# Optimization experiments

Measured on AMD Instinct MI355X. Metric: run time of the kernel, lower is better.

Reference implementation:

```python
import jax, jax.numpy as jnp
import numpy as np

B, S, D = 2, 2048, 1024
H = 16
HD = D // H

def setup_inputs() -> dict:
    key = jax.random.key(0)
    ks = jax.random.split(key, 9)
    s = 1.0 / np.sqrt(D)
    return {
        "x": jax.random.normal(ks[0], (B, S, D), dtype=jnp.float32),
        "Wq": jax.random.normal(ks[1], (D, D), dtype=jnp.float32) * s,
        "bq": jnp.zeros((D,), dtype=jnp.float32),
        "Wk": jax.random.normal(ks[2], (D, D), dtype=jnp.float32) * s,
        "bk": jnp.zeros((D,), dtype=jnp.float32),
        "Wv": jax.random.normal(ks[3], (D, D), dtype=jnp.float32) * s,
        "bv": jnp.zeros((D,), dtype=jnp.float32),
        "Wo": jax.random.normal(ks[4], (D, D), dtype=jnp.float32) * s,
        "bo": jnp.zeros((D,), dtype=jnp.float32),
    }

def reference(x, Wq, bq, Wk, bk, Wv, bv, Wo, bo):
    b, s, d = x.shape
    # torch Linear: y = x @ W.T + b
    def proj(W, bias):
        y = jnp.einsum('bsd,ed->bse', x, W) + bias
        return y.reshape(b, s, H, HD).transpose(0, 2, 1, 3)  # [b,h,s,hd]
    Q = proj(Wq, bq)
    K = proj(Wk, bk)
    V = proj(Wv, bv)
    scale = 1.0 / jnp.sqrt(jnp.float32(HD))
    scores = jnp.einsum('bhqd,bhkd->bhqk', Q, K) * scale  # [b,h,s,s]
    attn = jax.nn.softmax(scores, axis=-1)
    out = jnp.einsum('bhqk,bhkd->bhqd', attn, V)  # [b,h,s,hd]
    out = out.transpose(0, 2, 1, 3).reshape(b, s, d)
    return jnp.einsum('bsd,ed->bse', out, Wo) + bo
```

## Files before the change

kernel.cpp:

```cpp
#include <hip/hip_runtime.h>
#include <stdint.h>


typedef __bf16 bf16x8 __attribute__((ext_vector_type(8)));
typedef float  f32x4  __attribute__((ext_vector_type(4)));
typedef unsigned short u16x8 __attribute__((ext_vector_type(8)));

#define LOG2E 1.44269504088896f
#define FIXED_MAX_BITS 14.4269504088896f

__device__ __forceinline__ unsigned short f2bf(float f) {
    union { float f; unsigned u; } v; v.f = f;
    unsigned r = v.u + 0x7FFFu + ((v.u >> 16) & 1u);
    return (unsigned short)(r >> 16);
}
__device__ __forceinline__ float bf2f(unsigned short u) {
    union { unsigned u; float f; } v; v.u = (unsigned)u << 16; return v.f;
}

__device__ __forceinline__ float exp2_fast(float x) {
#if __has_builtin(__builtin_amdgcn_exp2f)
    return __builtin_amdgcn_exp2f(x);
#else
    return __expf(x * 0.69314718056f);
#endif
}

__device__ __forceinline__ void glds16(const void* g, void* l) {
    __builtin_amdgcn_global_load_lds(
        (__attribute__((address_space(1))) void*)(g),
        (__attribute__((address_space(3))) void*)(l),
        16, 0, 0);
}

__global__ __launch_bounds__(256) void cvt_all(
    const float* __restrict__ x,  const float* __restrict__ Wq,
    const float* __restrict__ Wk, const float* __restrict__ Wv,
    const float* __restrict__ Wo,
    unsigned short* __restrict__ xb,  unsigned short* __restrict__ Wqb,
    unsigned short* __restrict__ Wkb, unsigned short* __restrict__ Wvb,
    unsigned short* __restrict__ Wob)
{
    const int stride = gridDim.x * blockDim.x;
    for (int i = blockIdx.x * blockDim.x + threadIdx.x; i < 2097152; i += stride) {
        const float* src; unsigned short* dst; int j;
        if (i < 1048576) { src = x; dst = xb; j = i; }
        else {
            int t = (i - 1048576) >> 18; j = (i - 1048576) & 262143;
            src = (t == 0) ? Wq : (t == 1) ? Wk : (t == 2) ? Wv : Wo;
            dst = (t == 0) ? Wqb : (t == 1) ? Wkb : (t == 2) ? Wvb : Wob;
        }
        float4 v = ((const float4*)src)[j];
        ushort4 o;
        o.x = f2bf(v.x); o.y = f2bf(v.y); o.z = f2bf(v.z); o.w = f2bf(v.w);
        ((ushort4*)dst)[j] = o;
    }
}

template <int MODE>
__global__ __launch_bounds__(256) void gemm_bt(
    const unsigned short* __restrict__ A,
    const unsigned short* __restrict__ W0,
    const unsigned short* __restrict__ W1,
    const unsigned short* __restrict__ W2,
    const float* __restrict__ b0,
    const float* __restrict__ b1,
    const float* __restrict__ b2,
    unsigned short* __restrict__ outQ,
    unsigned short* __restrict__ outK,
    unsigned short* __restrict__ outV,
    float* __restrict__ outF)
{
    constexpr int BM = (MODE == 0) ? 128 : 64;
    constexpr int FM = BM / 32;
    constexpr int RA = BM / 32;

    __shared__ __attribute__((aligned(16))) unsigned short As[BM * 64];
    __shared__ __attribute__((aligned(16))) unsigned short Bs[128 * 64];

    const int tid  = threadIdx.x;
    const int lane = tid & 63;
    const int wid  = tid >> 6;
    const int quad = lane >> 4;
    const int l16  = lane & 15;

    const int m0 = blockIdx.x * BM;

    const unsigned short* W;
    const float* bias;
    int proj, n0;
    if (MODE == 0) {
        proj = blockIdx.y >> 3;
        n0   = (blockIdx.y & 7) * 128;
        W    = (proj == 0) ? W0 : (proj == 1) ? W1 : W2;
        bias = (proj == 0) ? b0 : (proj == 1) ? b1 : b2;
    } else {
        proj = 0;
        n0   = blockIdx.y * 128;
        W    = W0;
        bias = b0;
    }

    const int wm = (wid >> 1) * (BM / 2);
    const int wn = (wid & 1) * 64;

    f32x4 acc[FM][4];
#pragma unroll
    for (int i = 0; i < FM; ++i)
#pragma unroll
        for (int j = 0; j < 4; ++j)
            acc[i][j] = (f32x4){0.f, 0.f, 0.f, 0.f};

    char* AsB  = (char*)As;
    char* BsB  = (char*)Bs;
    char* ldsA = AsB + wid * 1024;
    char* ldsB = BsB + wid * 1024;

    for (int k0 = 0; k0 < 1024; k0 += 64) {
#pragma unroll
        for (int q = 0; q < RA; ++q) {
            int i   = q * 256 + tid;
            int row = i >> 3;
            int sc  = (i & 7) ^ (row & 7);
            glds16(A + (size_t)(m0 + row) * 1024 + k0 + sc * 8, ldsA + q * 4096);
        }
#pragma unroll
        for (int q = 0; q < 4; ++q) {
            int i   = q * 256 + tid;
            int row = i >> 3;
            int sc  = (i & 7) ^ (row & 7);
            glds16(W + (size_t)(n0 + row) * 1024 + k0 + sc * 8, ldsB + q * 4096);
        }
        __syncthreads();

#pragma unroll
        for (int kh = 0; kh < 2; ++kh) {
            bf16x8 af[FM], bfr[4];
#pragma unroll
            for (int t = 0; t < FM; ++t) {
                int r = wm + t * 16 + l16;
                int c = (kh * 4 + quad) ^ (r & 7);
                af[t] = *(const bf16x8*)(AsB + r * 128 + c * 16);
            }
#pragma unroll
            for (int t = 0; t < 4; ++t) {
                int r = wn + t * 16 + l16;
                int c = (kh * 4 + quad) ^ (r & 7);
                bfr[t] = *(const bf16x8*)(BsB + r * 128 + c * 16);
            }
#pragma unroll
            for (int i = 0; i < FM; ++i)
#pragma unroll
                for (int j = 0; j < 4; ++j)
                    acc[i][j] = __builtin_amdgcn_mfma_f32_16x16x32_bf16(
                        af[i], bfr[j], acc[i][j], 0, 0, 0);
        }
        __syncthreads();
    }

#pragma unroll
    for (int i = 0; i < FM; ++i) {
        const int mrow0 = m0 + wm + i * 16 + quad * 4;
#pragma unroll
        for (int j = 0; j < 4; ++j) {
            const int n  = n0 + wn + j * 16 + l16;
            const float bb = bias[n];
            if (MODE == 1) {
#pragma unroll
                for (int r = 0; r < 4; ++r)
                    outF[(size_t)(mrow0 + r) * 1024 + n] = acc[i][j][r] + bb;
            } else {
                const int h = n >> 6, hd = n & 63;
                if (proj == 2) {
                    const int b = mrow0 >> 11, s = mrow0 & 2047;
                    ushort4 pk;
                    pk.x = f2bf(acc[i][j][0] + bb);
                    pk.y = f2bf(acc[i][j][1] + bb);
                    pk.z = f2bf(acc[i][j][2] + bb);
                    pk.w = f2bf(acc[i][j][3] + bb);
                    *(ushort4*)(outV + ((size_t)((b * 16 + h) * 64 + hd)) * 2048 + s) = pk;
                } else {
                    unsigned short* dst = (proj == 0) ? outQ : outK;
                    const float scl = (proj == 0) ? (0.125f * LOG2E) : 1.0f;
#pragma unroll
                    for (int r = 0; r < 4; ++r) {
                        const int m = mrow0 + r;
                        const int b = m >> 11, s = m & 2047;
                        dst[((size_t)((b * 16 + h) * 2048 + s)) * 64 + hd] =
                            f2bf((acc[i][j][r] + bb) * scl);
                    }
                }
            }
        }
    }
}

__global__ __launch_bounds__(256, 4) void attn_kernel(
    const unsigned short* __restrict__ Qb,
    const unsigned short* __restrict__ Kb,
    const unsigned short* __restrict__ Vtb,
    unsigned short* __restrict__ OP,
    float* __restrict__ LS)
{
    __shared__ __attribute__((aligned(16))) unsigned short Ks[128 * 64];
    __shared__ __attribute__((aligned(16))) unsigned short Vs[2 * 64 * 64];

    const int tid  = threadIdx.x;
    const int lane = tid & 63;
    const int wid  = tid >> 6;
    const int quad = lane >> 4;
    const int l16  = lane & 15;
    const int l7   = l16 & 7;

    const int half = blockIdx.x & 1;
    const int q0   = (blockIdx.x >> 1) * 128 + wid * 32;
    const int hb   = blockIdx.y;
    const int bq   = hb >> 4, hh = hb & 15;

    const unsigned short* Qh  = Qb  + (size_t)hb * 2048 * 64;
    const unsigned short* Kh  = Kb  + (size_t)hb * 2048 * 64;
    const unsigned short* Vth = Vtb + (size_t)hb * 64 * 2048;

    bf16x8 qf[2][2];
#pragma unroll
    for (int qt = 0; qt < 2; ++qt) {
        const unsigned short* qp = Qh + (size_t)(q0 + qt * 16 + l16) * 64 + quad * 8;
        qf[qt][0] = *(const bf16x8*)(qp);
        qf[qt][1] = *(const bf16x8*)(qp + 32);
    }

    f32x4 o[4][2];
#pragma unroll
    for (int ht = 0; ht < 4; ++ht)
#pragma unroll
        for (int qt = 0; qt < 2; ++qt)
            o[ht][qt] = (f32x4){0.f, 0.f, 0.f, 0.f};
    float lsum[2] = {0.f, 0.f};

    char* KsB  = (char*)Ks;
    char* ldsK = KsB + wid * 1024;

    const int base_row = 8 * (l16 >> 2) + (l16 & 3);
    const int kp0 = ((quad) ^ l7) * 16;
    const int kp1 = ((4 + quad) ^ l7) * 16;
    const int vrow = l16 * 128;

    const int kc0 = half * 1024;
    for (int kc = kc0; kc < kc0 + 1024; kc += 128) {
#pragma unroll
        for (int q = 0; q < 4; ++q) {
            int i   = q * 256 + tid;
            int row = i >> 3;
            int g   = (row & 3) | (((row >> 3) & 1) << 2);
            int ch  = (i & 7) ^ g;
            glds16(Kh + (size_t)(kc + row) * 64 + ch * 8, ldsK + q * 4096);
        }
#pragma unroll
        for (int sub = 0; sub < 2; ++sub)
#pragma unroll
            for (int q = 0; q < 2; ++q) {
                int i   = q * 256 + tid;
                int row = i >> 3;
                int ch  = (i & 7) ^ (row & 7);
                glds16(Vth + (size_t)row * 2048 + kc + sub * 64 + ch * 8,
                       (char*)Vs + sub * 8192 + wid * 1024 + q * 4096);
            }
        __syncthreads();

#pragma unroll
        for (int st32 = 0; st32 < 4; ++st32) {
            const char* krb = KsB + (st32 * 32 + base_row) * 128;
            bf16x8 kf00 = *(const bf16x8*)(krb + kp0);
            bf16x8 kf01 = *(const bf16x8*)(krb + kp1);
            bf16x8 kf10 = *(const bf16x8*)(krb + 512 + kp0);
            bf16x8 kf11 = *(const bf16x8*)(krb + 512 + kp1);

            const f32x4 mi = (f32x4){-FIXED_MAX_BITS, -FIXED_MAX_BITS,
                                     -FIXED_MAX_BITS, -FIXED_MAX_BITS};
            f32x4 s00 = mi, s01 = mi, s10 = mi, s11 = mi;
            s00 = __builtin_amdgcn_mfma_f32_16x16x32_bf16(kf00, qf[0][0], s00, 0, 0, 0);
            s00 = __builtin_amdgcn_mfma_f32_16x16x32_bf16(kf01, qf[0][1], s00, 0, 0, 0);
            s01 = __builtin_amdgcn_mfma_f32_16x16x32_bf16(kf10, qf[0][0], s01, 0, 0, 0);
            s01 = __builtin_amdgcn_mfma_f32_16x16x32_bf16(kf11, qf[0][1], s01, 0, 0, 0);
            s10 = __builtin_amdgcn_mfma_f32_16x16x32_bf16(kf00, qf[1][0], s10, 0, 0, 0);
            s10 = __builtin_amdgcn_mfma_f32_16x16x32_bf16(kf01, qf[1][1], s10, 0, 0, 0);
            s11 = __builtin_amdgcn_mfma_f32_16x16x32_bf16(kf10, qf[1][0], s11, 0, 0, 0);
            s11 = __builtin_amdgcn_mfma_f32_16x16x32_bf16(kf11, qf[1][1], s11, 0, 0, 0);

            bf16x8 p8[2];
#pragma unroll
            for (int qt = 0; qt < 2; ++qt) {
                const f32x4 sA = qt ? s10 : s00;
                const f32x4 sB = qt ? s11 : s01;
                float e0 = exp2_fast(sA[0]), e1 = exp2_fast(sA[1]);
                float e2 = exp2_fast(sA[2]), e3 = exp2_fast(sA[3]);
                float e4 = exp2_fast(sB[0]), e5 = exp2_fast(sB[1]);
                float e6 = exp2_fast(sB[2]), e7 = exp2_fast(sB[3]);
                lsum[qt] += ((e0 + e1) + (e2 + e3)) + ((e4 + e5) + (e6 + e7));
                u16x8 up;
                up[0] = f2bf(e0); up[1] = f2bf(e1); up[2] = f2bf(e2); up[3] = f2bf(e3);
                up[4] = f2bf(e4); up[5] = f2bf(e5); up[6] = f2bf(e6); up[7] = f2bf(e7);
                p8[qt] = __builtin_bit_cast(bf16x8, up);
            }

            const int voff = (st32 >> 1) * 8192 + vrow
                           + ((((st32 & 1) * 4 + quad) ^ l7) * 16);
#pragma unroll
            for (int ht = 0; ht < 4; ++ht) {
                const bf16x8 vf = *(const bf16x8*)((char*)Vs + voff + ht * 2048);
                o[ht][0] = __builtin_amdgcn_mfma_f32_16x16x32_bf16(vf, p8[0], o[ht][0], 0, 0, 0);
                o[ht][1] = __builtin_amdgcn_mfma_f32_16x16x32_bf16(vf, p8[1], o[ht][1], 0, 0, 0);
            }
        }
        __syncthreads();
    }

    float lt[2];
#pragma unroll
    for (int qt = 0; qt < 2; ++qt) {
        float s = lsum[qt];
        s += __shfl_xor(s, 16);
        s += __shfl_xor(s, 32);
        lt[qt] = s;
    }

    unsigned short* OPh = OP + (size_t)half * 4096 * 1024;
#pragma unroll
    for (int qt = 0; qt < 2; ++qt) {
        const size_t row = (size_t)(bq * 2048 + q0 + qt * 16 + l16);
#pragma unroll
        for (int ht = 0; ht < 4; ++ht) {
            ushort4 pk;
            pk.x = f2bf(o[ht][qt][0]);
            pk.y = f2bf(o[ht][qt][1]);
            pk.z = f2bf(o[ht][qt][2]);
            pk.w = f2bf(o[ht][qt][3]);
            *(ushort4*)(OPh + row * 1024 + hh * 64 + ht * 16 + quad * 4) = pk;
        }
    }
    if (quad == 0) {
        LS[half * 65536 + hb * 2048 + q0 + l16]      = lt[0];
        LS[half * 65536 + hb * 2048 + q0 + 16 + l16] = lt[1];
    }
}

__global__ __launch_bounds__(256) void attn_reduce(
    const unsigned short* __restrict__ OP,
    const float* __restrict__ LS,
    unsigned short* __restrict__ attnb)
{
    const size_t idx = ((size_t)blockIdx.x * 256 + threadIdx.x) * 8;
    const int row = (int)(idx >> 10);
    const int col = (int)(idx & 1023);
    const int bh  = ((row >> 11) << 4) + (col >> 6);
    const int q   = row & 2047;
    const float l = LS[bh * 2048 + q] + LS[65536 + bh * 2048 + q];
    const float rl = 1.0f / l;

    ushort4 a0 = *(const ushort4*)(OP + idx);
    ushort4 a1 = *(const ushort4*)(OP + idx + 4);
    ushort4 b0 = *(const ushort4*)(OP + 4194304 + idx);
    ushort4 b1 = *(const ushort4*)(OP + 4194304 + idx + 4);
    ushort4 o0, o1;
    o0.x = f2bf((bf2f(a0.x) + bf2f(b0.x)) * rl);
    o0.y = f2bf((bf2f(a0.y) + bf2f(b0.y)) * rl);
    o0.z = f2bf((bf2f(a0.z) + bf2f(b0.z)) * rl);
    o0.w = f2bf((bf2f(a0.w) + bf2f(b0.w)) * rl);
    o1.x = f2bf((bf2f(a1.x) + bf2f(b1.x)) * rl);
    o1.y = f2bf((bf2f(a1.y) + bf2f(b1.y)) * rl);
    o1.z = f2bf((bf2f(a1.z) + bf2f(b1.z)) * rl);
    o1.w = f2bf((bf2f(a1.w) + bf2f(b1.w)) * rl);
    *(ushort4*)(attnb + idx)     = o0;
    *(ushort4*)(attnb + idx + 4) = o1;
}

extern "C" void kernel_launch(void* const* d_in, const int* in_sizes, int n_in,
                              void* d_out, int out_size, void* d_ws, size_t ws_size,
                              hipStream_t stream) {
    (void)in_sizes; (void)n_in; (void)out_size; (void)ws_size;

    const float* x  = (const float*)d_in[0];
    const float* Wq = (const float*)d_in[1];
    const float* bq = (const float*)d_in[2];
    const float* Wk = (const float*)d_in[3];
    const float* bk = (const float*)d_in[4];
    const float* Wv = (const float*)d_in[5];
    const float* bv = (const float*)d_in[6];
    const float* Wo = (const float*)d_in[7];
    const float* bo = (const float*)d_in[8];

    char* ws = (char*)d_ws;
    const size_t MB = 1024 * 1024;
    unsigned short* xb    = (unsigned short*)(ws + 0);
    unsigned short* Wqb   = (unsigned short*)(ws + 8  * MB);
    unsigned short* Wkb   = (unsigned short*)(ws + 10 * MB);
    unsigned short* Wvb   = (unsigned short*)(ws + 12 * MB);
    unsigned short* Wob   = (unsigned short*)(ws + 14 * MB);
    unsigned short* Qb    = (unsigned short*)(ws + 16 * MB);
    unsigned short* Kb    = (unsigned short*)(ws + 24 * MB);
    unsigned short* Vtb   = (unsigned short*)(ws + 32 * MB);
    unsigned short* attnb = (unsigned short*)(ws + 40 * MB);
    unsigned short* OP    = (unsigned short*)(ws + 48 * MB);
    float*          LSb   = (float*)(ws + 64 * MB);

    cvt_all<<<dim3(1024), dim3(256), 0, stream>>>(
        x, Wq, Wk, Wv, Wo, xb, Wqb, Wkb, Wvb, Wob);

    gemm_bt<0><<<dim3(32, 24), dim3(256), 0, stream>>>(
        xb, Wqb, Wkb, Wvb, bq, bk, bv, Qb, Kb, Vtb, nullptr);

    attn_kernel<<<dim3(32, 32), dim3(256), 0, stream>>>(Qb, Kb, Vtb, OP, LSb);

    attn_reduce<<<dim3(2048), dim3(256), 0, stream>>>(OP, LSb, attnb);

    gemm_bt<1><<<dim3(64, 8), dim3(256), 0, stream>>>(
        attnb, Wob, nullptr, nullptr, bo, nullptr, nullptr,
        nullptr, nullptr, nullptr, (float*)d_out);
}
```

Measured before the change: 199.1 us.

## Fuse x fp32-to-bf16 conversion into QKV GEMM and use packed bf16 converts

Drops the separate conversion of x to bf16. The QKV GEMM now loads fp32 x directly, converts it in registers and stores it to LDS, which removes one full write and read of the activation through HBM. It also replaces scalar bf16 rounding with the packed cvt_pk_bf16_f32 builtin where available, in the attention softmax, in the epilogues and in the reduce. In exchange, the A operand in the QKV GEMM is now loaded synchronously through registers instead of async global_load_lds, and each x tile is converted repeatedly, once per N-block (24 column blocks).

```diff
diff --git a/kernel.cpp b/kernel.cpp
--- a/kernel.cpp
+++ b/kernel.cpp
@@ -3,8 +3,9 @@
 
 
 typedef __bf16 bf16x8 __attribute__((ext_vector_type(8)));
+typedef __bf16 bf16x2 __attribute__((ext_vector_type(2)));
 typedef float  f32x4  __attribute__((ext_vector_type(4)));
-typedef unsigned short u16x8 __attribute__((ext_vector_type(8)));
+typedef unsigned int u32x4v __attribute__((ext_vector_type(4)));
 
 #define LOG2E 1.44269504088896f
 #define FIXED_MAX_BITS 14.4269504088896f
@@ -16,6 +17,14 @@
 }
 __device__ __forceinline__ float bf2f(unsigned short u) {
     union { unsigned u; float f; } v; v.u = (unsigned)u << 16; return v.f;
+}
+
+__device__ __forceinline__ unsigned cvtpk(float a, float b) {
+#if __has_builtin(__builtin_amdgcn_cvt_pk_bf16_f32)
+    return __builtin_bit_cast(unsigned, __builtin_amdgcn_cvt_pk_bf16_f32(a, b));
+#else
+    return (unsigned)f2bf(a) | ((unsigned)f2bf(b) << 16);
+#endif
 }
 
 __device__ __forceinline__ float exp2_fast(float x) {
@@ -33,33 +42,29 @@
         16, 0, 0);
 }
 
-__global__ __launch_bounds__(256) void cvt_all(
-    const float* __restrict__ x,  const float* __restrict__ Wq,
-    const float* __restrict__ Wk, const float* __restrict__ Wv,
-    const float* __restrict__ Wo,
-    unsigned short* __restrict__ xb,  unsigned short* __restrict__ Wqb,
-    unsigned short* __restrict__ Wkb, unsigned short* __restrict__ Wvb,
-    unsigned short* __restrict__ Wob)
+__global__ __launch_bounds__(256) void cvt_w(
+    const float* __restrict__ Wq, const float* __restrict__ Wk,
+    const float* __restrict__ Wv, const float* __restrict__ Wo,
+    unsigned short* __restrict__ Wqb, unsigned short* __restrict__ Wkb,
+    unsigned short* __restrict__ Wvb, unsigned short* __restrict__ Wob)
 {
     const int stride = gridDim.x * blockDim.x;
-    for (int i = blockIdx.x * blockDim.x + threadIdx.x; i < 2097152; i += stride) {
-        const float* src; unsigned short* dst; int j;
-        if (i < 1048576) { src = x; dst = xb; j = i; }
-        else {
-            int t = (i - 1048576) >> 18; j = (i - 1048576) & 262143;
-            src = (t == 0) ? Wq : (t == 1) ? Wk : (t == 2) ? Wv : Wo;
-            dst = (t == 0) ? Wqb : (t == 1) ? Wkb : (t == 2) ? Wvb : Wob;
-        }
+    for (int i = blockIdx.x * blockDim.x + threadIdx.x; i < 1048576; i += stride) {
+        int t = i >> 18, j = i & 262143;
+        const float* src = (t == 0) ? Wq : (t == 1) ? Wk : (t == 2) ? Wv : Wo;
+        unsigned short* dst = (t == 0) ? Wqb : (t == 1) ? Wkb : (t == 2) ? Wvb : Wob;
         float4 v = ((const float4*)src)[j];
-        ushort4 o;
-        o.x = f2bf(v.x); o.y = f2bf(v.y); o.z = f2bf(v.z); o.w = f2bf(v.w);
-        ((ushort4*)dst)[j] = o;
+        uint2 o;
+        o.x = cvtpk(v.x, v.y);
+        o.y = cvtpk(v.z, v.w);
+        ((uint2*)dst)[j] = o;
     }
 }
 
 template <int MODE>
 __global__ __launch_bounds__(256) void gemm_bt(
     const unsigned short* __restrict__ A,
+    const float* __restrict__ A32,
     const unsigned short* __restrict__ W0,
     const unsigned short* __restrict__ W1,
     const unsigned short* __restrict__ W2,
@@ -117,12 +122,30 @@
     char* ldsB = BsB + wid * 1024;
 
     for (int k0 = 0; k0 < 1024; k0 += 64) {
-#pragma unroll
-        for (int q = 0; q < RA; ++q) {
-            int i   = q * 256 + tid;
-            int row = i >> 3;
-            int sc  = (i & 7) ^ (row & 7);
-            glds16(A + (size_t)(m0 + row) * 1024 + k0 + sc * 8, ldsA + q * 4096);
+        if (MODE == 0) {
+#pragma unroll
+            for (int q = 0; q < RA; ++q) {
+                int i   = q * 256 + tid;
+                int row = i >> 3;
+                int sc  = (i & 7) ^ (row & 7);
+                const float* src = A32 + (size_t)(m0 + row) * 1024 + k0 + sc * 8;
+                float4 v0 = *(const float4*)(src);
+                float4 v1 = *(const float4*)(src + 4);
+                u32x4v pk;
+                pk.x = cvtpk(v0.x, v0.y);
+                pk.y = cvtpk(v0.z, v0.w);
+                pk.z = cvtpk(v1.x, v1.y);
+                pk.w = cvtpk(v1.z, v1.w);
+                *(u32x4v*)(AsB + i * 16) = pk;
+            }
+        } else {
+#pragma unroll
+            for (int q = 0; q < RA; ++q) {
+                int i   = q * 256 + tid;
+                int row = i >> 3;
+                int sc  = (i & 7) ^ (row & 7);
+                glds16(A + (size_t)(m0 + row) * 1024 + k0 + sc * 8, ldsA + q * 4096);
+            }
         }
 #pragma unroll
         for (int q = 0; q < 4; ++q) {
@@ -173,12 +196,10 @@
                 const int h = n >> 6, hd = n & 63;
                 if (proj == 2) {
                     const int b = mrow0 >> 11, s = mrow0 & 2047;
-                    ushort4 pk;
-                    pk.x = f2bf(acc[i][j][0] + bb);
-                    pk.y = f2bf(acc[i][j][1] + bb);
-                    pk.z = f2bf(acc[i][j][2] + bb);
-                    pk.w = f2bf(acc[i][j][3] + bb);
-                    *(ushort4*)(outV + ((size_t)((b * 16 + h) * 64 + hd)) * 2048 + s) = pk;
+                    uint2 pk;
+                    pk.x = cvtpk(acc[i][j][0] + bb, acc[i][j][1] + bb);
+                    pk.y = cvtpk(acc[i][j][2] + bb, acc[i][j][3] + bb);
+                    *(uint2*)(outV + ((size_t)((b * 16 + h) * 64 + hd)) * 2048 + s) = pk;
                 } else {
                     unsigned short* dst = (proj == 0) ? outQ : outK;
                     const float scl = (proj == 0) ? (0.125f * LOG2E) : 1.0f;
@@ -297,9 +318,11 @@
                 float e4 = exp2_fast(sB[0]), e5 = exp2_fast(sB[1]);
                 float e6 = exp2_fast(sB[2]), e7 = exp2_fast(sB[3]);
                 lsum[qt] += ((e0 + e1) + (e2 + e3)) + ((e4 + e5) + (e6 + e7));
-                u16x8 up;
-                up[0] = f2bf(e0); up[1] = f2bf(e1); up[2] = f2bf(e2); up[3] = f2bf(e3);
-                up[4] = f2bf(e4); up[5] = f2bf(e5); up[6] = f2bf(e6); up[7] = f2bf(e7);
+                u32x4v up;
+                up.x = cvtpk(e0, e1);
+                up.y = cvtpk(e2, e3);
+                up.z = cvtpk(e4, e5);
+                up.w = cvtpk(e6, e7);
                 p8[qt] = __builtin_bit_cast(bf16x8, up);
             }
 
@@ -330,12 +353,10 @@
         const size_t row = (size_t)(bq * 2048 + q0 + qt * 16 + l16);
 #pragma unroll
         for (int ht = 0; ht < 4; ++ht) {
-            ushort4 pk;
-            pk.x = f2bf(o[ht][qt][0]);
-            pk.y = f2bf(o[ht][qt][1]);
-            pk.z = f2bf(o[ht][qt][2]);
-            pk.w = f2bf(o[ht][qt][3]);
-            *(ushort4*)(OPh + row * 1024 + hh * 64 + ht * 16 + quad * 4) = pk;
+            uint2 pk;
+            pk.x = cvtpk(o[ht][qt][0], o[ht][qt][1]);
+            pk.y = cvtpk(o[ht][qt][2], o[ht][qt][3]);
+            *(uint2*)(OPh + row * 1024 + hh * 64 + ht * 16 + quad * 4) = pk;
         }
     }
     if (quad == 0) {
@@ -361,17 +382,12 @@
     ushort4 a1 = *(const ushort4*)(OP + idx + 4);
     ushort4 b0 = *(const ushort4*)(OP + 4194304 + idx);
     ushort4 b1 = *(const ushort4*)(OP + 4194304 + idx + 4);
-    ushort4 o0, o1;
-    o0.x = f2bf((bf2f(a0.x) + bf2f(b0.x)) * rl);
-    o0.y = f2bf((bf2f(a0.y) + bf2f(b0.y)) * rl);
-    o0.z = f2bf((bf2f(a0.z) + bf2f(b0.z)) * rl);
-    o0.w = f2bf((bf2f(a0.w) + bf2f(b0.w)) * rl);
-    o1.x = f2bf((bf2f(a1.x) + bf2f(b1.x)) * rl);
-    o1.y = f2bf((bf2f(a1.y) + bf2f(b1.y)) * rl);
-    o1.z = f2bf((bf2f(a1.z) + bf2f(b1.z)) * rl);
-    o1.w = f2bf((bf2f(a1.w) + bf2f(b1.w)) * rl);
-    *(ushort4*)(attnb + idx)     = o0;
-    *(ushort4*)(attnb + idx + 4) = o1;
+    u32x4v o;
+    o.x = cvtpk((bf2f(a0.x) + bf2f(b0.x)) * rl, (bf2f(a0.y) + bf2f(b0.y)) * rl);
+    o.y = cvtpk((bf2f(a0.z) + bf2f(b0.z)) * rl, (bf2f(a0.w) + bf2f(b0.w)) * rl);
+    o.z = cvtpk((bf2f(a1.x) + bf2f(b1.x)) * rl, (bf2f(a1.y) + bf2f(b1.y)) * rl);
+    o.w = cvtpk((bf2f(a1.z) + bf2f(b1.z)) * rl, (bf2f(a1.w) + bf2f(b1.w)) * rl);
+    *(u32x4v*)(attnb + idx) = o;
 }
 
 extern "C" void kernel_launch(void* const* d_in, const int* in_sizes, int n_in,
@@ -391,7 +407,6 @@
 
     char* ws = (char*)d_ws;
     const size_t MB = 1024 * 1024;
-    unsigned short* xb    = (unsigned short*)(ws + 0);
     unsigned short* Wqb   = (unsigned short*)(ws + 8  * MB);
     unsigned short* Wkb   = (unsigned short*)(ws + 10 * MB);
     unsigned short* Wvb   = (unsigned short*)(ws + 12 * MB);
@@ -403,17 +418,17 @@
     unsigned short* OP    = (unsigned short*)(ws + 48 * MB);
     float*          LSb   = (float*)(ws + 64 * MB);
 
-    cvt_all<<<dim3(1024), dim3(256), 0, stream>>>(
-        x, Wq, Wk, Wv, Wo, xb, Wqb, Wkb, Wvb, Wob);
+    cvt_w<<<dim3(512), dim3(256), 0, stream>>>(
+        Wq, Wk, Wv, Wo, Wqb, Wkb, Wvb, Wob);
 
     gemm_bt<0><<<dim3(32, 24), dim3(256), 0, stream>>>(
-        xb, Wqb, Wkb, Wvb, bq, bk, bv, Qb, Kb, Vtb, nullptr);
+        nullptr, x, Wqb, Wkb, Wvb, bq, bk, bv, Qb, Kb, Vtb, nullptr);
 
     attn_kernel<<<dim3(32, 32), dim3(256), 0, stream>>>(Qb, Kb, Vtb, OP, LSb);
 
     attn_reduce<<<dim3(2048), dim3(256), 0, stream>>>(OP, LSb, attnb);
 
     gemm_bt<1><<<dim3(64, 8), dim3(256), 0, stream>>>(
-        attnb, Wob, nullptr, nullptr, bo, nullptr, nullptr,
+        attnb, nullptr, Wob, nullptr, nullptr, bo, nullptr, nullptr,
         nullptr, nullptr, nullptr, (float*)d_out);
 }
```

Result: slower. 218.0 us (+9.5%).
